# Performance work log

Hardware: AMD Instinct MI355X
Metric: run time of the kernel (lower is better)

Reference implementation:

```python
import jax, jax.numpy as jnp
import numpy as np

N_NODES = 262144
N_EDGES = 4194304
N_GRAPHS = 1024
IN_DIM = 10
HIDDEN = 32


def setup_inputs() -> dict:
    key = jax.random.key(0)
    ks = jax.random.split(key, 8)
    x = jax.random.normal(ks[0], (N_NODES, IN_DIM), dtype=jnp.float32)
    edge_index = jax.random.randint(ks[1], (2, N_EDGES), 0, N_NODES, dtype=jnp.int64)
    batch = jnp.sort(jax.random.randint(ks[2], (N_NODES,), 0, N_GRAPHS, dtype=jnp.int64))
    W1 = jax.random.normal(ks[3], (IN_DIM, HIDDEN), dtype=jnp.float32) * (1.0 / np.sqrt(IN_DIM))
    b1 = jnp.zeros((HIDDEN,), dtype=jnp.float32)
    W2 = jax.random.normal(ks[4], (HIDDEN, HIDDEN), dtype=jnp.float32) * (1.0 / np.sqrt(HIDDEN))
    b2 = jnp.zeros((HIDDEN,), dtype=jnp.float32)
    Wlin = jax.random.normal(ks[5], (HIDDEN, 1), dtype=jnp.float32) * (1.0 / np.sqrt(HIDDEN))
    blin = jnp.zeros((1,), dtype=jnp.float32)
    return {"x": x, "edge_index": edge_index, "batch": batch,
            "W1": W1, "b1": b1, "W2": W2, "b2": b2, "Wlin": Wlin, "blin": blin}


def _gcn_norm(edge_index, num_nodes):
    # PyG GCNConv default: add self-loops, symmetric normalization.
    loop = jnp.arange(num_nodes, dtype=edge_index.dtype)
    src = jnp.concatenate([edge_index[0], loop])
    dst = jnp.concatenate([edge_index[1], loop])
    deg = jax.ops.segment_sum(jnp.ones_like(dst, dtype=jnp.float32), dst,
                              num_segments=num_nodes)
    dinv = jnp.where(deg > 0, jax.lax.rsqrt(deg), 0.0)
    norm = dinv[src] * dinv[dst]  # [E+N]
    return src, dst, norm


def _gcn_conv(x, W, b, src, dst, norm, num_nodes):
    h = x @ W                              # [N, out]
    msg = h[src] * norm[:, None]           # gather + scale  [E+N, out]
    out = jax.ops.segment_sum(msg, dst, num_segments=num_nodes)  # scatter-add
    return out + b


def reference(x, edge_index, batch, W1, b1, W2, b2, Wlin, blin):
    n = x.shape[0]
    src, dst, norm = _gcn_norm(edge_index, n)
    h = jax.nn.relu(_gcn_conv(x, W1, b1, src, dst, norm, n))
    h = jax.nn.relu(_gcn_conv(h, W2, b2, src, dst, norm, n))
    # global_mean_pool over graph ids
    sums = jax.ops.segment_sum(h, batch, num_segments=N_GRAPHS)
    cnt = jax.ops.segment_sum(jnp.ones((n,), dtype=h.dtype), batch,
                              num_segments=N_GRAPHS)
    pooled = sums / jnp.maximum(cnt, 1.0)[:, None]   # [G, hidden]
    return (pooled @ Wlin + blin).squeeze(-1)        # [G]
```

## Files before the change

kernel.cpp:

```cpp
#include <hip/hip_runtime.h>
#include <stdint.h>

#define N_NODES 262144
#define N_EDGES 4194304
#define N_GRAPHS 1024
#define IN_DIM 10
#define HIDDEN 32
#define NBUCKET 1024
#define NSUB 8
#define CAP_SUB 704
#define BROW (NSUB * CAP_SUB)
#define STG_CAP BROW
#define S_EDGES 16384
#define PA_BLOCKS (N_EDGES / S_EDGES)
#define PA_THREADS 512

__device__ __forceinline__ float fatomic_add(float* p, float v) {
    return unsafeAtomicAdd(p, v);
}

__device__ __forceinline__ uint16_t f2bf(float f) {
    uint32_t u = __float_as_uint(f);
    u = (u + 0x7FFF + ((u >> 16) & 1)) >> 16;
    return (uint16_t)u;
}
__device__ __forceinline__ float bf_lo(uint32_t w) { return __uint_as_float(w << 16); }
__device__ __forceinline__ float bf_hi(uint32_t w) { return __uint_as_float(w & 0xFFFF0000u); }


__global__ __launch_bounds__(PA_THREADS) void passA(const int* __restrict__ src,
                                                    const int* __restrict__ dst,
                                                    int* __restrict__ bcnt,
                                                    uint32_t* __restrict__ arena) {
    __shared__ int hist[NBUCKET];
    __shared__ int cur[NBUCKET];
    int blk = blockIdx.x, t = threadIdx.x;
    int j = blk & (NSUB - 1);
    size_t e0 = (size_t)blk * S_EDGES;

    for (int k = t; k < NBUCKET; k += PA_THREADS) hist[k] = 0;
    __syncthreads();

    const int4* dp = reinterpret_cast<const int4*>(dst + e0);
    const int4* sp = reinterpret_cast<const int4*>(src + e0);

    for (int k = t; k < S_EDGES / 4; k += PA_THREADS) {
        int4 d4 = dp[k];
        atomicAdd(&hist[d4.x >> 8], 1);
        atomicAdd(&hist[d4.y >> 8], 1);
        atomicAdd(&hist[d4.z >> 8], 1);
        atomicAdd(&hist[d4.w >> 8], 1);
    }
    __syncthreads();

    for (int k = t; k < NBUCKET; k += PA_THREADS) {
        int h = hist[k];
        cur[k] = (h > 0) ? atomicAdd(&bcnt[(k * NSUB + j) * 16], h) : 0;
    }
    __syncthreads();

    for (int k = t; k < S_EDGES / 4; k += PA_THREADS) {
        int4 d4 = dp[k];
        int4 s4 = sp[k];
        {
            int d = d4.x, b = d >> 8;
            int pos = atomicAdd(&cur[b], 1);
            if (pos < CAP_SUB)
                arena[(size_t)(b * NSUB + j) * CAP_SUB + pos] = ((uint32_t)(d & 255) << 18) | (uint32_t)s4.x;
        }
        {
            int d = d4.y, b = d >> 8;
            int pos = atomicAdd(&cur[b], 1);
            if (pos < CAP_SUB)
                arena[(size_t)(b * NSUB + j) * CAP_SUB + pos] = ((uint32_t)(d & 255) << 18) | (uint32_t)s4.y;
        }
        {
            int d = d4.z, b = d >> 8;
            int pos = atomicAdd(&cur[b], 1);
            if (pos < CAP_SUB)
                arena[(size_t)(b * NSUB + j) * CAP_SUB + pos] = ((uint32_t)(d & 255) << 18) | (uint32_t)s4.z;
        }
        {
            int d = d4.w, b = d >> 8;
            int pos = atomicAdd(&cur[b], 1);
            if (pos < CAP_SUB)
                arena[(size_t)(b * NSUB + j) * CAP_SUB + pos] = ((uint32_t)(d & 255) << 18) | (uint32_t)s4.w;
        }
    }
}


__global__ void bucket_sort(uint32_t* __restrict__ arena, const int* __restrict__ bcnt,
                            const float* __restrict__ x, float* __restrict__ dinv,
                            uint32_t* __restrict__ binfo, uint16_t* __restrict__ xs) {
    __shared__ uint32_t stg[STG_CAP];
    __shared__ int scnt[NSUB];
    __shared__ int h[256];
    __shared__ int cur[256];
    __shared__ float dsh[256];
    int b = blockIdx.x, t = threadIdx.x;
    int base = b * 256;
    if (t < NSUB) {
        int c = bcnt[(b * NSUB + t) * 16];
        scnt[t] = (c > CAP_SUB) ? CAP_SUB : c;
    }
    h[t] = 0;
    __syncthreads();
    int off = 0;
    #pragma unroll
    for (int j = 0; j < NSUB; ++j) {
        int len = scnt[j];
        const uint32_t* sp = arena + (size_t)(b * NSUB + j) * CAP_SUB;
        for (int k = t; k < len; k += 256) stg[off + k] = sp[k];
        off += len;
    }
    int nb = off;
    __syncthreads();
    for (int k = t; k < nb; k += 256) atomicAdd(&h[stg[k] >> 18], 1);
    __syncthreads();
    int myh = h[t];
    #pragma unroll
    for (int o = 1; o < 256; o <<= 1) {
        int v = (t >= o) ? h[t - o] : 0;
        __syncthreads();
        h[t] += v;
        __syncthreads();
    }
    int excl = h[t] - myh;
    binfo[base + t] = ((uint32_t)excl << 13) | (uint32_t)myh;
    float dv = rsqrtf(1.0f + (float)myh);
    dinv[base + t] = dv;
    dsh[t] = dv;
    cur[t] = excl;
    __syncthreads();
    uint32_t* wp = arena + (size_t)b * BROW;
    for (int k = t; k < nb; k += 256) {
        uint32_t w = stg[k];
        int d = w >> 18;
        int pos = atomicAdd(&cur[d], 1);
        wp[pos] = w & 0x3FFFF;
    }
    for (int idx = t; idx < 256 * 16; idx += 256) {
        int n = idx >> 4, k = idx & 15;
        float val = (k < IN_DIM) ? x[(size_t)(base + n) * IN_DIM + k] * dsh[n] : 0.0f;
        xs[(size_t)(base + n) * 16 + k] = f2bf(val);
    }
}


__global__ void agg1_dense1(const uint16_t* __restrict__ xs, const uint32_t* __restrict__ arena,
                            const uint32_t* __restrict__ binfo, const float* __restrict__ dinv,
                            const float* __restrict__ W1, const float* __restrict__ b1,
                            uint16_t* __restrict__ zs) {
    __shared__ float ash[64 * 12];
    __shared__ float w[IN_DIM * HIDDEN];
    int t = threadIdx.x;
    int base = blockIdx.x * 64;
    for (int j = t; j < IN_DIM * HIDDEN; j += 256) w[j] = W1[j];

    int lane = t & 63;
    int nib = (t >> 6) * 16 + (lane >> 2);
    int n = base + nib;
    int q = lane & 1, g = (lane >> 1) & 1;
    uint32_t info = binfo[n];
    int beg = (int)(info >> 13), len = (int)(info & 0x1FFF);
    const uint32_t* ep = arena + (size_t)(n >> 8) * BROW + beg;
    const uint4* Xv = reinterpret_cast<const uint4*>(xs);
    float a[8];
    #pragma unroll
    for (int j = 0; j < 8; ++j) a[j] = 0.0f;
    if (g == 0) {
        uint4 v = Xv[(size_t)n * 2 + q];
        a[0] += bf_lo(v.x); a[1] += bf_hi(v.x);
        a[2] += bf_lo(v.y); a[3] += bf_hi(v.y);
        a[4] += bf_lo(v.z); a[5] += bf_hi(v.z);
        a[6] += bf_lo(v.w); a[7] += bf_hi(v.w);
    }
    for (int i = g; i < len; i += 2) {
        int si = (int)ep[i];
        uint4 v = Xv[(size_t)si * 2 + q];
        a[0] += bf_lo(v.x); a[1] += bf_hi(v.x);
        a[2] += bf_lo(v.y); a[3] += bf_hi(v.y);
        a[4] += bf_lo(v.z); a[5] += bf_hi(v.z);
        a[6] += bf_lo(v.w); a[7] += bf_hi(v.w);
    }
    #pragma unroll
    for (int j = 0; j < 8; ++j) a[j] += __shfl_xor(a[j], 2);
    if (g == 0) {
        if (q == 0) {
            #pragma unroll
            for (int j = 0; j < 8; ++j) ash[nib * 12 + j] = a[j];
        } else {
            #pragma unroll
            for (int j = 0; j < 4; ++j) ash[nib * 12 + 8 + j] = a[j];
        }
    }
    __syncthreads();

    int dn_i = t >> 2, c0 = (t & 3) * 8;
    int node = base + dn_i;
    float s[8];
    #pragma unroll
    for (int j = 0; j < 8; ++j) s[j] = 0.0f;
    #pragma unroll
    for (int k = 0; k < IN_DIM; ++k) {
        float ak = ash[dn_i * 12 + k];
        #pragma unroll
        for (int j = 0; j < 8; ++j) s[j] += ak * w[k * HIDDEN + c0 + j];
    }
    float dv = dinv[node];
    uint32_t pk[4];
    #pragma unroll
    for (int j = 0; j < 4; ++j) {
        float v0 = fmaxf(dv * s[2 * j] + b1[c0 + 2 * j], 0.0f) * dv;
        float v1 = fmaxf(dv * s[2 * j + 1] + b1[c0 + 2 * j + 1], 0.0f) * dv;
        pk[j] = (uint32_t)f2bf(v0) | ((uint32_t)f2bf(v1) << 16);
    }
    reinterpret_cast<uint4*>(zs)[(size_t)node * 4 + (t & 3)] =
        make_uint4(pk[0], pk[1], pk[2], pk[3]);
}


__global__ void agg2_dense2_pool(const uint16_t* __restrict__ zs, const uint32_t* __restrict__ arena,
                                 const uint32_t* __restrict__ binfo, const float* __restrict__ dinv,
                                 const float* __restrict__ W2, const float* __restrict__ b2,
                                 const int* __restrict__ batch, float* __restrict__ pooled) {
    __shared__ float vsh[64 * 33];
    __shared__ float w[HIDDEN * HIDDEN];
    __shared__ int bsh[64];
    int t = threadIdx.x;
    int base = blockIdx.x * 64;
    for (int j = t; j < HIDDEN * HIDDEN; j += 256) w[j] = W2[j];
    if (t < 64) bsh[t] = batch[base + t];

    int lane = t & 63;
    int nib = (t >> 6) * 16 + (lane >> 2);
    int n = base + nib;
    int q = lane & 3;
    uint32_t info = binfo[n];
    int beg = (int)(info >> 13), len = (int)(info & 0x1FFF);
    const uint32_t* ep = arena + (size_t)(n >> 8) * BROW + beg;
    const uint4* Zv = reinterpret_cast<const uint4*>(zs);
    float a[8];
    {
        uint4 v = Zv[(size_t)n * 4 + q];
        a[0] = bf_lo(v.x); a[1] = bf_hi(v.x);
        a[2] = bf_lo(v.y); a[3] = bf_hi(v.y);
        a[4] = bf_lo(v.z); a[5] = bf_hi(v.z);
        a[6] = bf_lo(v.w); a[7] = bf_hi(v.w);
    }
    for (int i = 0; i < len; ++i) {
        int si = (int)ep[i];
        uint4 v = Zv[(size_t)si * 4 + q];
        a[0] += bf_lo(v.x); a[1] += bf_hi(v.x);
        a[2] += bf_lo(v.y); a[3] += bf_hi(v.y);
        a[4] += bf_lo(v.z); a[5] += bf_hi(v.z);
        a[6] += bf_lo(v.w); a[7] += bf_hi(v.w);
    }
    #pragma unroll
    for (int j = 0; j < 8; ++j) vsh[nib * 33 + q * 8 + j] = a[j];
    __syncthreads();

    int dn_i = t >> 2, c0 = (t & 3) * 8;
    int node = base + dn_i;
    float s[8];
    #pragma unroll
    for (int j = 0; j < 8; ++j) s[j] = 0.0f;
    #pragma unroll
    for (int k = 0; k < HIDDEN; ++k) {
        float ak = vsh[dn_i * 33 + k];
        #pragma unroll
        for (int j = 0; j < 8; ++j) s[j] += ak * w[k * HIDDEN + c0 + j];
    }
    float dv = dinv[node];
    float v[8];
    #pragma unroll
    for (int j = 0; j < 8; ++j) v[j] = fmaxf(dv * s[j] + b2[c0 + j], 0.0f);
    __syncthreads();
    #pragma unroll
    for (int j = 0; j < 8; ++j) vsh[dn_i * 33 + c0 + j] = v[j];
    __syncthreads();

    int col = t & 31, seg = t >> 5;
    int r0 = seg * 8;
    float run = vsh[r0 * 33 + col];
    int cur = bsh[r0];
    #pragma unroll
    for (int j = 1; j < 8; ++j) {
        int bg = bsh[r0 + j];
        float vv = vsh[(r0 + j) * 33 + col];
        if (bg == cur) run += vv;
        else {
            fatomic_add(&pooled[(size_t)cur * HIDDEN + col], run);
            run = vv;
            cur = bg;
        }
    }
    fatomic_add(&pooled[(size_t)cur * HIDDEN + col], run);
}


__global__ void final_k(const float* __restrict__ pooled, const int* __restrict__ batch,
                        const float* __restrict__ Wlin, const float* __restrict__ blin,
                        float* __restrict__ out) {
    int g = blockIdx.x * blockDim.x + threadIdx.x;
    if (g < N_GRAPHS) {
        int lo = 0, hi = N_NODES;
        while (lo < hi) { int mid = (lo + hi) >> 1; if (batch[mid] < g) lo = mid + 1; else hi = mid; }
        int first = lo;
        lo = 0; hi = N_NODES;
        while (lo < hi) { int mid = (lo + hi) >> 1; if (batch[mid] <= g) lo = mid + 1; else hi = mid; }
        float cc = (float)(lo - first);
        if (cc < 1.0f) cc = 1.0f;
        float s = 0.0f;
        #pragma unroll
        for (int c = 0; c < HIDDEN; ++c) s += pooled[(size_t)g * HIDDEN + c] * Wlin[c];
        out[g] = s / cc + blin[0];
    }
}


extern "C" void kernel_launch(void* const* d_in, const int* in_sizes, int n_in,
                              void* d_out, int out_size, void* d_ws, size_t ws_size,
                              hipStream_t stream) {
    const float* x     = (const float*)d_in[0];
    const int*   ei    = (const int*)d_in[1];
    const int*   batch = (const int*)d_in[2];
    const float* W1    = (const float*)d_in[3];
    const float* b1    = (const float*)d_in[4];
    const float* W2    = (const float*)d_in[5];
    const float* b2    = (const float*)d_in[6];
    const float* Wlin  = (const float*)d_in[7];
    const float* blin  = (const float*)d_in[8];
    float* out = (float*)d_out;

    const int* src = ei;
    const int* dst = ei + N_EDGES;

    const size_t N = N_NODES;
    float*    F      = (float*)d_ws;
    uint16_t* zs     = (uint16_t*)F;
    uint16_t* xs     = (uint16_t*)(F + 8 * N);
    float*    dinv   = F + 16 * N;
    uint32_t* binfo  = (uint32_t*)(dinv + N);
    int*      bcnt   = (int*)(binfo + N);
    float*    pooled = (float*)(bcnt + NBUCKET * NSUB * 16);
    uint32_t* arena  = (uint32_t*)(pooled + (size_t)N_GRAPHS * HIDDEN);

    size_t zbytes = ((size_t)NBUCKET * NSUB * 16 + (size_t)N_GRAPHS * HIDDEN) * sizeof(int);
    hipMemsetAsync(bcnt, 0, zbytes, stream);

    passA<<<PA_BLOCKS, PA_THREADS, 0, stream>>>(src, dst, bcnt, arena);
    bucket_sort<<<NBUCKET, 256, 0, stream>>>(arena, bcnt, x, dinv, binfo, xs);
    agg1_dense1<<<N_NODES / 64, 256, 0, stream>>>(xs, arena, binfo, dinv, W1, b1, zs);
    agg2_dense2_pool<<<N_NODES / 64, 256, 0, stream>>>(zs, arena, binfo, dinv, W2, b2, batch, pooled);
    final_k<<<(N_GRAPHS + 255) / 256, 256, 0, stream>>>(pooled, batch, Wlin, blin, out);
}
```

Baseline: 248.8 us.

## Sort nodes by degree within 64-node groups to balance wavefront gather loops

bucket_sort now counting-sorts each 64-node group by in-degree and writes a permuted info array holding the local node index, edge offset and capped length. The two aggregation kernels read this array, so each wavefront's 16 nodes have similar degrees. The goal is less divergence and idle lanes in the per-node neighbor gather loops. The cost is an extra shared histogram, scan and atomics in bucket_sort. Degrees are clamped to 1023 in the packed length field.

```diff
diff --git a/kernel.cpp b/kernel.cpp
--- a/kernel.cpp
+++ b/kernel.cpp
@@ -92,12 +92,13 @@
 
 __global__ void bucket_sort(uint32_t* __restrict__ arena, const int* __restrict__ bcnt,
                             const float* __restrict__ x, float* __restrict__ dinv,
-                            uint32_t* __restrict__ binfo, uint16_t* __restrict__ xs) {
+                            uint32_t* __restrict__ binfo2, uint16_t* __restrict__ xs) {
     __shared__ uint32_t stg[STG_CAP];
     __shared__ int scnt[NSUB];
     __shared__ int h[256];
     __shared__ int cur[256];
     __shared__ float dsh[256];
+    __shared__ int dh[256];
     int b = blockIdx.x, t = threadIdx.x;
     int base = b * 256;
     if (t < NSUB) {
@@ -105,6 +106,7 @@
         scnt[t] = (c > CAP_SUB) ? CAP_SUB : c;
     }
     h[t] = 0;
+    dh[t] = 0;
     __syncthreads();
     int off = 0;
     #pragma unroll
@@ -127,12 +129,31 @@
         __syncthreads();
     }
     int excl = h[t] - myh;
-    binfo[base + t] = ((uint32_t)excl << 13) | (uint32_t)myh;
     float dv = rsqrtf(1.0f + (float)myh);
     dinv[base + t] = dv;
     dsh[t] = dv;
     cur[t] = excl;
-    __syncthreads();
+    int g64 = t >> 6, lane = t & 63;
+    int dbin = (myh > 63) ? 63 : myh;
+    atomicAdd(&dh[g64 * 64 + dbin], 1);
+    __syncthreads();
+    {
+        int v = dh[g64 * 64 + lane];
+        int inc = v;
+        #pragma unroll
+        for (int o = 1; o < 64; o <<= 1) {
+            int u = __shfl_up(inc, o);
+            if (lane >= o) inc += u;
+        }
+        dh[g64 * 64 + lane] = inc - v;
+    }
+    __syncthreads();
+    {
+        int slot = atomicAdd(&dh[g64 * 64 + dbin], 1);
+        int lc = (myh > 1023) ? 1023 : myh;
+        binfo2[base + g64 * 64 + slot] =
+            ((uint32_t)lane << 23) | ((uint32_t)excl << 10) | (uint32_t)lc;
+    }
     uint32_t* wp = arena + (size_t)b * BROW;
     for (int k = t; k < nb; k += 256) {
         uint32_t w = stg[k];
@@ -149,7 +170,7 @@
 
 
 __global__ void agg1_dense1(const uint16_t* __restrict__ xs, const uint32_t* __restrict__ arena,
-                            const uint32_t* __restrict__ binfo, const float* __restrict__ dinv,
+                            const uint32_t* __restrict__ binfo2, const float* __restrict__ dinv,
                             const float* __restrict__ W1, const float* __restrict__ b1,
                             uint16_t* __restrict__ zs) {
     __shared__ float ash[64 * 12];
@@ -158,12 +179,13 @@
     int base = blockIdx.x * 64;
     for (int j = t; j < IN_DIM * HIDDEN; j += 256) w[j] = W1[j];
 
-    int lane = t & 63;
-    int nib = (t >> 6) * 16 + (lane >> 2);
+    int idx = t >> 2;
+    uint32_t wrd = binfo2[base + idx];
+    int nib = (int)(wrd >> 23);
+    int beg = (int)((wrd >> 10) & 0x1FFF);
+    int len = (int)(wrd & 0x3FF);
     int n = base + nib;
-    int q = lane & 1, g = (lane >> 1) & 1;
-    uint32_t info = binfo[n];
-    int beg = (int)(info >> 13), len = (int)(info & 0x1FFF);
+    int q = t & 1, g = (t >> 1) & 1;
     const uint32_t* ep = arena + (size_t)(n >> 8) * BROW + beg;
     const uint4* Xv = reinterpret_cast<const uint4*>(xs);
     float a[8];
@@ -208,12 +230,12 @@
         #pragma unroll
         for (int j = 0; j < 8; ++j) s[j] += ak * w[k * HIDDEN + c0 + j];
     }
-    float dv = dinv[node];
+    float dvv = dinv[node];
     uint32_t pk[4];
     #pragma unroll
     for (int j = 0; j < 4; ++j) {
-        float v0 = fmaxf(dv * s[2 * j] + b1[c0 + 2 * j], 0.0f) * dv;
-        float v1 = fmaxf(dv * s[2 * j + 1] + b1[c0 + 2 * j + 1], 0.0f) * dv;
+        float v0 = fmaxf(dvv * s[2 * j] + b1[c0 + 2 * j], 0.0f) * dvv;
+        float v1 = fmaxf(dvv * s[2 * j + 1] + b1[c0 + 2 * j + 1], 0.0f) * dvv;
         pk[j] = (uint32_t)f2bf(v0) | ((uint32_t)f2bf(v1) << 16);
     }
     reinterpret_cast<uint4*>(zs)[(size_t)node * 4 + (t & 3)] =
@@ -222,7 +244,7 @@
 
 
 __global__ void agg2_dense2_pool(const uint16_t* __restrict__ zs, const uint32_t* __restrict__ arena,
-                                 const uint32_t* __restrict__ binfo, const float* __restrict__ dinv,
+                                 const uint32_t* __restrict__ binfo2, const float* __restrict__ dinv,
                                  const float* __restrict__ W2, const float* __restrict__ b2,
                                  const int* __restrict__ batch, float* __restrict__ pooled) {
     __shared__ float vsh[64 * 33];
@@ -233,12 +255,13 @@
     for (int j = t; j < HIDDEN * HIDDEN; j += 256) w[j] = W2[j];
     if (t < 64) bsh[t] = batch[base + t];
 
-    int lane = t & 63;
-    int nib = (t >> 6) * 16 + (lane >> 2);
+    int idx = t >> 2;
+    uint32_t wrd = binfo2[base + idx];
+    int nib = (int)(wrd >> 23);
+    int beg = (int)((wrd >> 10) & 0x1FFF);
+    int len = (int)(wrd & 0x3FF);
     int n = base + nib;
-    int q = lane & 3;
-    uint32_t info = binfo[n];
-    int beg = (int)(info >> 13), len = (int)(info & 0x1FFF);
+    int q = t & 3;
     const uint32_t* ep = arena + (size_t)(n >> 8) * BROW + beg;
     const uint4* Zv = reinterpret_cast<const uint4*>(zs);
     float a[8];
@@ -272,10 +295,10 @@
         #pragma unroll
         for (int j = 0; j < 8; ++j) s[j] += ak * w[k * HIDDEN + c0 + j];
     }
-    float dv = dinv[node];
+    float dvv = dinv[node];
     float v[8];
     #pragma unroll
-    for (int j = 0; j < 8; ++j) v[j] = fmaxf(dv * s[j] + b2[c0 + j], 0.0f);
+    for (int j = 0; j < 8; ++j) v[j] = fmaxf(dvv * s[j] + b2[c0 + j], 0.0f);
     __syncthreads();
     #pragma unroll
     for (int j = 0; j < 8; ++j) vsh[dn_i * 33 + c0 + j] = v[j];
@@ -342,8 +365,8 @@
     uint16_t* zs     = (uint16_t*)F;
     uint16_t* xs     = (uint16_t*)(F + 8 * N);
     float*    dinv   = F + 16 * N;
-    uint32_t* binfo  = (uint32_t*)(dinv + N);
-    int*      bcnt   = (int*)(binfo + N);
+    uint32_t* binfo2 = (uint32_t*)(dinv + N);
+    int*      bcnt   = (int*)(binfo2 + N);
     float*    pooled = (float*)(bcnt + NBUCKET * NSUB * 16);
     uint32_t* arena  = (uint32_t*)(pooled + (size_t)N_GRAPHS * HIDDEN);
 
@@ -351,8 +374,8 @@
     hipMemsetAsync(bcnt, 0, zbytes, stream);
 
     passA<<<PA_BLOCKS, PA_THREADS, 0, stream>>>(src, dst, bcnt, arena);
-    bucket_sort<<<NBUCKET, 256, 0, stream>>>(arena, bcnt, x, dinv, binfo, xs);
-    agg1_dense1<<<N_NODES / 64, 256, 0, stream>>>(xs, arena, binfo, dinv, W1, b1, zs);
-    agg2_dense2_pool<<<N_NODES / 64, 256, 0, stream>>>(zs, arena, binfo, dinv, W2, b2, batch, pooled);
+    bucket_sort<<<NBUCKET, 256, 0, stream>>>(arena, bcnt, x, dinv, binfo2, xs);
+    agg1_dense1<<<N_NODES / 64, 256, 0, stream>>>(xs, arena, binfo2, dinv, W1, b1, zs);
+    agg2_dense2_pool<<<N_NODES / 64, 256, 0, stream>>>(zs, arena, binfo2, dinv, W2, b2, batch, pooled);
     final_k<<<(N_GRAPHS + 255) / 256, 256, 0, stream>>>(pooled, batch, Wlin, blin, out);
 }
```

New measurement: 247.3 us. No clear change (-0.6%).
